# Optimization experiments

Measured on AMD Instinct MI355X. Metric: run time of the kernel, lower is better.

## Reference

```python
import jax, jax.numpy as jnp
import numpy as np

BINS = 10
MOMENTUM = 0.5
N = 16_777_216  # flat element / class count


def setup_inputs() -> dict:
    key = jax.random.key(0)
    k1, k2 = jax.random.split(key)
    pred = jax.random.normal(k1, (N,), dtype=jnp.float32)
    target = jax.random.uniform(k2, (N,), dtype=jnp.float32)
    return {"pred": pred, "target": target}


def reference(pred, target):
    # edges = linspace(0,1,bins+1) with last edge nudged up by 1e-6
    edges = jnp.linspace(0.0, 1.0, BINS + 1).at[-1].add(1e-6)

    # gradient magnitude g = |sigmoid(pred).detach() - target|
    p_sig = jax.lax.stop_gradient(jax.nn.sigmoid(pred))
    g = jnp.abs(p_sig - target)

    valid = jnp.isfinite(g) & jnp.isfinite(target)
    total_samples = jnp.sum(valid).astype(jnp.float32)

    # torch.bucketize(g, edges) with right=False == searchsorted left
    inds = jnp.searchsorted(edges, g, side="left")  # values in [0, BINS]
    # bincount(inds, minlength=BINS) -> histogram over BINS+1 buckets,
    # counting only valid elements (scatter-add)
    sample_in_bin = jnp.zeros(BINS + 1, jnp.float32).at[inds].add(
        valid.astype(jnp.float32)
    )

    # EMA: stored acc_sum is never updated in the torch module (stays zeros),
    # so the local acc_sum = momentum*0 + (1-momentum)*counts each call.
    acc_sum_state = jnp.zeros(BINS + 1, jnp.float32)
    acc_sum = MOMENTUM * acc_sum_state + (1.0 - MOMENTUM) * sample_in_bin

    total_positives = jnp.sum(acc_sum)
    total_negatives = total_samples - total_positives  # computed pre-clamp
    total_positives = jnp.maximum(total_positives, 1.0)

    pred_det = jax.lax.stop_gradient(pred)
    ratio = total_negatives / total_positives
    weights = jnp.where(target > pred_det, ratio, 1.0)
    weights = jnp.where(valid, weights, 0.0)  # weights only defined on valid

    # F.cross_entropy with 1-D logits [C], float (soft-label) target [C],
    # per-class weight [C], reduction='mean' on a single unbatched sample:
    # loss = -sum_c w_c * t_c * log_softmax(pred)_c
    logp = jax.nn.log_softmax(pred)
    loss = -jnp.sum(weights * target * logp)
    return loss
```

## Files before the change

kernel.cpp:

```cpp
#include <hip/hip_runtime.h>
#include <math.h>


#define NT 256
#define UN 4
#define CHUNK_F4 (NT * UN)
#define MAXNB 4096
#define SHIFTC 16.0f

typedef float vf4 __attribute__((ext_vector_type(4)));

__device__ __forceinline__ float min4(vf4 t) { return fminf(fminf(t.x, t.y), fminf(t.z, t.w)); }
__device__ __forceinline__ float max4(vf4 t) { return fmaxf(fmaxf(t.x, t.y), fmaxf(t.z, t.w)); }

struct Acc5 { float S, At, Bt, Agt, Bgt; };

__device__ __forceinline__ void acc_elem(Acc5& a, float p, float t) {
    const float L2E = 1.4426950408889634f;
    a.S += exp2f(fmaf(p, L2E, -SHIFTC));
    float ts = (t > p) ? t : 0.0f;
    a.Bt += t;
    a.Bgt += ts;
    a.At  = fmaf(t,  p, a.At);
    a.Agt = fmaf(ts, p, a.Agt);
}

__device__ __forceinline__ void acc_group(Acc5& a, vf4 p, vf4 t) {
    acc_elem(a, p.x, t.x); acc_elem(a, p.y, t.y);
    acc_elem(a, p.z, t.z); acc_elem(a, p.w, t.w);
}

__device__ __forceinline__ void hist_fix(float& hd, float p, float t) {
    const float L2E = 1.4426950408889634f;
    if (isfinite(t)) {
        float sig = 1.0f / (1.0f + exp2f(-p * L2E));
        float g = fabsf(sig - t);
        if (g > 1.000001f) hd += 1.0f;
    }
}

__device__ __forceinline__ void fix_group(float& hd, vf4 p, vf4 t) {
    hist_fix(hd, p.x, t.x); hist_fix(hd, p.y, t.y);
    hist_fix(hd, p.z, t.z); hist_fix(hd, p.w, t.w);
}

__device__ __forceinline__ void proc_group(Acc5& a, float& hd, vf4 P, vf4 T) {
    acc_group(a, P, T);
    if (!(min4(T) >= 0.0f && max4(T) <= 1.0f)) fix_group(hd, P, T);
}

__device__ __forceinline__ void block_reduce_write(float* v, float* out8) {
    #pragma unroll
    for (int off = 32; off > 0; off >>= 1) {
        #pragma unroll
        for (int q = 0; q < 6; q++) v[q] += __shfl_down(v[q], off);
    }
    __shared__ float red[NT / 64][6];
    int wave = threadIdx.x >> 6;
    int lane = threadIdx.x & 63;
    if (lane == 0) {
        #pragma unroll
        for (int q = 0; q < 6; q++) red[wave][q] = v[q];
    }
    __syncthreads();
    if (threadIdx.x == 0) {
        float s[6];
        #pragma unroll
        for (int q = 0; q < 6; q++) s[q] = red[0][q];
        #pragma unroll
        for (int w = 1; w < NT / 64; w++)
            #pragma unroll
            for (int q = 0; q < 6; q++) s[q] += red[w][q];
        #pragma unroll
        for (int q = 0; q < 6; q++) out8[q] = s[q];
    }
}

__global__ __launch_bounds__(NT) void ghm_pass1(const float* __restrict__ pred,
                                                const float* __restrict__ targ,
                                                float* __restrict__ ws,
                                                int n, int nchunks) {
    const vf4* p4 = (const vf4*)pred;
    const vf4* t4 = (const vf4*)targ;
    int tid = threadIdx.x;
    int n4 = n >> 2;

    Acc5 a = {0.f, 0.f, 0.f, 0.f, 0.f};
    float hd = 0.0f;

    for (int c = blockIdx.x; c < nchunks; c += gridDim.x) {
        int base = c * CHUNK_F4 + tid;
        vf4 P[UN], T[UN];
        #pragma unroll
        for (int u = 0; u < UN; u++) P[u] = __builtin_nontemporal_load(&p4[base + u * NT]);
        #pragma unroll
        for (int u = 0; u < UN; u++) T[u] = __builtin_nontemporal_load(&t4[base + u * NT]);
        #pragma unroll
        for (int u = 0; u < UN; u++) proc_group(a, hd, P[u], T[u]);
    }

    for (int j = nchunks * CHUNK_F4 + blockIdx.x * NT + tid; j < n4;
         j += gridDim.x * NT) {
        vf4 P = __builtin_nontemporal_load(&p4[j]);
        vf4 T = __builtin_nontemporal_load(&t4[j]);
        proc_group(a, hd, P, T);
    }

    if (blockIdx.x == 0 && tid == 0) {
        for (int j = n4 << 2; j < n; j++) {
            float p = pred[j], t = targ[j];
            acc_elem(a, p, t);
            if (!(t >= 0.0f && t <= 1.0f)) hist_fix(hd, p, t);
        }
    }

    float v[6] = {a.S, a.At, a.Bt, a.Agt, a.Bgt, hd};
    block_reduce_write(v, &ws[(size_t)blockIdx.x * 8]);
}

__global__ __launch_bounds__(NT) void ghm_pass2(const float* __restrict__ ws,
                                                float* __restrict__ out, int nb, int n) {
    float v[6] = {0.f, 0.f, 0.f, 0.f, 0.f, 0.f};
    for (int i = threadIdx.x; i < nb; i += NT) {
        const float* p = &ws[(size_t)i * 8];
        #pragma unroll
        for (int q = 0; q < 6; q++) v[q] += p[q];
    }
    __shared__ float res[8];
    block_reduce_write(v, res);
    if (threadIdx.x == 0) {
        float S = res[0], At = res[1], Bt = res[2], Agt = res[3], Bgt = res[4], hd = res[5];
        float cnt  = (float)n;
        float hcnt = cnt - hd;
        float tp0  = 0.5f * hcnt;
        float tneg = cnt - tp0;
        float ratio = tneg / fmaxf(tp0, 1.0f);
        float A = ratio * Agt + (At - Agt);
        float B = ratio * Bgt + (Bt - Bgt);
        float lse = (log2f(S) + SHIFTC) * 0.69314718055994531f;
        out[0] = lse * B - A;
    }
}

extern "C" void kernel_launch(void* const* d_in, const int* in_sizes, int n_in,
                              void* d_out, int out_size, void* d_ws, size_t ws_size,
                              hipStream_t stream) {
    const float* pred = (const float*)d_in[0];
    const float* targ = (const float*)d_in[1];
    float* out = (float*)d_out;
    float* ws = (float*)d_ws;
    int n = in_sizes[0];
    int n4 = n >> 2;
    int nchunks = n4 / CHUNK_F4;

    int nb = nchunks < MAXNB ? (nchunks > 0 ? nchunks : 1) : MAXNB;
    size_t cap = ws_size / (8 * sizeof(float));
    if ((size_t)nb > cap) nb = (int)cap;
    if (nb < 1) nb = 1;

    ghm_pass1<<<nb, NT, 0, stream>>>(pred, targ, ws, n, nchunks);
    ghm_pass2<<<1, NT, 0, stream>>>(ws, out, nb, n);
}
```

Baseline: 141.9 us.

## Software-pipeline pass1 loads with double buffers and contiguous per-block chunks

Each block now processes a contiguous range of chunks and double-buffers the pred/target loads, issuing the next chunk's loads before processing the current one. The grid is fixed at 1024 blocks instead of up to 4096. The aim is to hide global memory latency with more bytes in flight per thread. In exchange, register pressure goes up, which can lower occupancy, and the smaller grid may leave less wave-level parallelism to hide latency.

```diff
diff --git a/kernel.cpp b/kernel.cpp
--- a/kernel.cpp
+++ b/kernel.cpp
@@ -5,7 +5,7 @@
 #define NT 256
 #define UN 4
 #define CHUNK_F4 (NT * UN)
-#define MAXNB 4096
+#define NBLK 1024
 #define SHIFTC 16.0f
 
 typedef float vf4 __attribute__((ext_vector_type(4)));
@@ -49,6 +49,23 @@
     if (!(min4(T) >= 0.0f && max4(T) <= 1.0f)) fix_group(hd, P, T);
 }
 
+#define LOAD_CHUNK(Pb, Tb, c)                                                   \
+    do {                                                                        \
+        int base_ = (c) * CHUNK_F4 + tid;                                       \
+        _Pragma("unroll")                                                       \
+        for (int u = 0; u < UN; u++)                                            \
+            Pb[u] = __builtin_nontemporal_load(&p4[base_ + u * NT]);            \
+        _Pragma("unroll")                                                       \
+        for (int u = 0; u < UN; u++)                                            \
+            Tb[u] = __builtin_nontemporal_load(&t4[base_ + u * NT]);            \
+    } while (0)
+
+#define PROC_CHUNK(Pb, Tb)                                                      \
+    do {                                                                        \
+        _Pragma("unroll")                                                       \
+        for (int u = 0; u < UN; u++) proc_group(a, hd, Pb[u], Tb[u]);           \
+    } while (0)
+
 __device__ __forceinline__ void block_reduce_write(float* v, float* out8) {
     #pragma unroll
     for (int off = 32; off > 0; off >>= 1) {
@@ -88,15 +105,25 @@
     Acc5 a = {0.f, 0.f, 0.f, 0.f, 0.f};
     float hd = 0.0f;
 
-    for (int c = blockIdx.x; c < nchunks; c += gridDim.x) {
-        int base = c * CHUNK_F4 + tid;
-        vf4 P[UN], T[UN];
-        #pragma unroll
-        for (int u = 0; u < UN; u++) P[u] = __builtin_nontemporal_load(&p4[base + u * NT]);
-        #pragma unroll
-        for (int u = 0; u < UN; u++) T[u] = __builtin_nontemporal_load(&t4[base + u * NT]);
-        #pragma unroll
-        for (int u = 0; u < UN; u++) proc_group(a, hd, P[u], T[u]);
+    int cpb = nchunks / gridDim.x;
+    int c0 = blockIdx.x * cpb;
+
+    vf4 PA[UN], TA[UN], PB[UN], TB[UN];
+    if (cpb > 0) {
+        LOAD_CHUNK(PA, TA, c0);
+        int k = 0;
+        for (; k + 2 <= cpb; k += 2) {
+            LOAD_CHUNK(PB, TB, c0 + k + 1);
+            PROC_CHUNK(PA, TA);
+            if (k + 2 < cpb) LOAD_CHUNK(PA, TA, c0 + k + 2);
+            PROC_CHUNK(PB, TB);
+        }
+        if (k < cpb) PROC_CHUNK(PA, TA);
+    }
+
+    for (int c = gridDim.x * cpb + blockIdx.x; c < nchunks; c += gridDim.x) {
+        LOAD_CHUNK(PA, TA, c);
+        PROC_CHUNK(PA, TA);
     }
 
     for (int j = nchunks * CHUNK_F4 + blockIdx.x * NT + tid; j < n4;
@@ -153,7 +180,7 @@
     int n4 = n >> 2;
     int nchunks = n4 / CHUNK_F4;
 
-    int nb = nchunks < MAXNB ? (nchunks > 0 ? nchunks : 1) : MAXNB;
+    int nb = NBLK;
     size_t cap = ws_size / (8 * sizeof(float));
     if ((size_t)nb > cap) nb = (int)cap;
     if (nb < 1) nb = 1;
```

Result: no change. 141.4 us (median of 2 runs) (-0.3%).
